# Optimization experiments

Hardware: AMD Instinct MI355X
Metric: run time of the kernel (lower is better)

## Reference

```python
import jax, jax.numpy as jnp
import numpy as np

B, T, D = 32, 1024, 1024  # batch, t_k (encoder steps), attn_sz == cell_state_sz


def setup_inputs() -> dict:
    key = jax.random.key(0)
    ks = jax.random.split(key, 7)
    scale = 1.0 / np.sqrt(D)
    return {
        "h_i": jax.random.normal(ks[0], (B, T, D), jnp.float32),
        "s_t": jax.random.normal(ks[1], (B, D), jnp.float32),
        "coverage": jax.random.uniform(ks[2], (B, T), jnp.float32),
        "W_h": jax.random.normal(ks[3], (D, D), jnp.float32) * scale,
        "W_s": jax.random.normal(ks[4], (D, D), jnp.float32) * scale,
        "b_s": jnp.zeros((D,), jnp.float32),
        "W_c": jax.random.normal(ks[5], (D,), jnp.float32) * scale,  # Dense(1 -> D) kernel
        "V_w": jax.random.normal(ks[6], (D,), jnp.float32) * scale,  # Dense(D -> 1) kernel
    }


def reference(h_i, s_t, coverage, W_h, W_s, b_s, W_c, V_w):
    # enc_features = W_h(h_i): (B, T, D)
    enc_features = jnp.einsum("btd,de->bte", h_i, W_h)
    # dec_features = W_s(s_t) broadcast over time: (B, 1, D)
    dec_features = (s_t @ W_s + b_s)[:, None, :]
    # coverage features: scalar coverage per step times (1->D) kernel
    cov_features = coverage[:, :, None] * W_c[None, None, :]
    features = enc_features + dec_features + cov_features
    # e_t = V(tanh(features)) squeezed to (B, T)
    e_t = jnp.einsum("btd,d->bt", jnp.tanh(features), V_w)
    a_t = jax.nn.softmax(e_t, axis=1)
    coverage_new = coverage + a_t
    # context = a_t @ h_i : (B, D)
    context_vector = jnp.einsum("bt,btd->bd", a_t, h_i)
    return context_vector, a_t, coverage_new
```

## Files before the change

### kernel.cpp

```cpp
#include <hip/hip_runtime.h>

#define B_ 32
#define T_ 1024
#define D_ 1024
#define M_ (B_ * T_)
#define NT_ 8
#define NT2 4
#define BM_ 128
#define BN_ 128
#define BK_ 64
#define NKT (D_ / BK_)
#define LSTR 72

#define FENCE_ALL() asm volatile("s_waitcnt vmcnt(0) lgkmcnt(0)" ::: "memory")

typedef __attribute__((ext_vector_type(8))) short short8;
typedef __attribute__((ext_vector_type(4))) float f32x4;

__device__ __forceinline__ unsigned f2bf(float f) {
    union { float f; unsigned u; } v; v.f = f;
    return (v.u + 0x7FFFu + ((v.u >> 16) & 1u)) >> 16;
}
__device__ __forceinline__ unsigned pack2(float a, float b) {
    return f2bf(a) | (f2bf(b) << 16);
}
__device__ __forceinline__ float bf2f(unsigned hi16) {
    union { unsigned u; float f; } v; v.u = hi16 << 16;
    return v.f;
}
__device__ __forceinline__ float fast_tanh(float x) {
    x = fminf(15.0f, fmaxf(-15.0f, x));
    float e = __expf(2.0f * x);
    return (e - 1.0f) * __fdividef(1.0f, e + 1.0f);
}

#define PREP_CONVH_BLKS 2048
#define PREP_CONVWT_BLKS 256
#define PREP_DEC_BLKS (B_ * 16)
__global__ __launch_bounds__(256) void prep_kernel(
    const float* __restrict__ h_i, uint4* __restrict__ h_bf4,
    const float* __restrict__ W_h, unsigned short* __restrict__ Wt,
    const float* __restrict__ s_t, const float* __restrict__ W_s,
    const float* __restrict__ b_s, float* __restrict__ dec_part)
{
    __shared__ float smem[64 * 65];
    const int bid = blockIdx.x;
    const int tid = threadIdx.x;
    if (bid < PREP_CONVH_BLKS) {
        const int idx = bid * 256 + tid;
        const int stride = PREP_CONVH_BLKS * 256;
        const int ngroups = M_ * D_ / 8;
        const float4* in4 = (const float4*)h_i;
        for (int g = idx; g < ngroups; g += stride) {
            const float4 a = in4[2 * g];
            const float4 b = in4[2 * g + 1];
            h_bf4[g] = make_uint4(pack2(a.x, a.y), pack2(a.z, a.w),
                                  pack2(b.x, b.y), pack2(b.z, b.w));
        }
    } else if (bid < PREP_CONVH_BLKS + PREP_CONVWT_BLKS) {
        const int tb = bid - PREP_CONVH_BLKS;
        float (*tile)[65] = (float (*)[65])smem;
        const int k0 = (tb & 15) * 64;
        const int n0 = (tb >> 4) * 64;
        const int tx = tid & 63, ty = tid >> 6;
#pragma unroll
        for (int r = 0; r < 16; ++r) {
            const int row = ty * 16 + r;
            tile[row][tx] = W_h[(size_t)(k0 + row) * D_ + n0 + tx];
        }
        __syncthreads();
#pragma unroll
        for (int r = 0; r < 16; ++r) {
            const int row = ty * 16 + r;
            Wt[(size_t)(n0 + row) * D_ + k0 + tx] = (unsigned short)f2bf(tile[tx][row]);
        }
    } else {
        const int db = bid - (PREP_CONVH_BLKS + PREP_CONVWT_BLKS);
        const int kc = db & 3;
        const int nc = (db >> 2) & 3;
        const int b  = db >> 4;
        const int d = nc * 256 + tid;
        const int k0 = kc * 256;
        float* s_lds = smem;
        s_lds[tid] = s_t[b * D_ + k0 + tid];
        __syncthreads();
        float acc = (kc == 0) ? b_s[d] : 0.f;
#pragma unroll 8
        for (int k = 0; k < 256; ++k) acc += s_lds[k] * W_s[(size_t)(k0 + k) * D_ + d];
        dec_part[kc * (B_ * D_) + b * D_ + d] = acc;
    }
}

__global__ __launch_bounds__(512, 2) void attn_gemm2(
    const unsigned short* __restrict__ h_bf, const unsigned short* __restrict__ wt_bf,
    const float* __restrict__ dec_part, const float* __restrict__ coverage,
    const float* __restrict__ W_c, const float* __restrict__ V_w,
    float* __restrict__ e_part)
{
    __shared__ __align__(16) unsigned short lds2[2][2][256 * 64];
    __shared__ float e_red[4][256];

    const int tid = threadIdx.x;
    const int nt2 = blockIdx.x >> 7;
    const int mt  = blockIdx.x & 127;
    const int m0 = mt * 256;
    const int n0 = nt2 * 256;
    const int bb = m0 >> 10;

    const int wave = tid >> 6;
    const int lane = tid & 63;
    const int wr = wave >> 2;
    const int wc = wave & 3;
    const int lr = lane & 15;
    const int lk = lane >> 4;

    f32x4 acc[8][4];
    const f32x4 fzero = {0.f, 0.f, 0.f, 0.f};
#pragma unroll
    for (int i = 0; i < 8; ++i)
#pragma unroll
        for (int j = 0; j < 4; ++j) acc[i][j] = fzero;

    const char* gA = (const char*)h_bf + (size_t)m0 * (D_ * 2);
    const char* gB = (const char*)wt_bf + (size_t)n0 * (D_ * 2);
    const int lrow8 = lane >> 3;
    const int scol = (((lane & 7) ^ lrow8) << 4);
    const int sw = (lr & 7) << 4;

#define GLOAD(mat, chunk, kt, buf)                                                 \
    {                                                                              \
        const int row_ = (chunk) * 8 + lrow8;                                      \
        const size_t goff_ = (size_t)row_ * (D_ * 2) + (size_t)(kt) * 128 + scol;  \
        __builtin_amdgcn_global_load_lds(                                          \
            (const __attribute__((address_space(1))) void*)(((mat) ? gB : gA) + goff_), \
            (__attribute__((address_space(3))) void*)((char*)lds2 +                \
                ((buf) * 2 + (mat)) * 32768 + (chunk) * 1024), 16, 0, 0);          \
    }
#define ST_BLO(buf, kt) { GLOAD(1, 2 * wave, kt, buf); GLOAD(1, 2 * wave + 1, kt, buf); }
#define ST_BHI(buf, kt) { GLOAD(1, 16 + 2 * wave, kt, buf); GLOAD(1, 16 + 2 * wave + 1, kt, buf); }
#define ST_AU(buf, kt, g)                                                          \
    { const int c_ = (wave < 4) ? ((g) * 4 + wave) : (16 + (g) * 4 + (wave - 4));  \
      GLOAD(0, c_, kt, buf); }

#define PH_BAR(N)                                                                  \
    asm volatile("s_waitcnt vmcnt(" #N ")" ::: "memory");                          \
    __builtin_amdgcn_s_barrier();                                                  \
    asm volatile("" ::: "memory")

#define LOADA(g)                                                                   \
    _Pragma("unroll")                                                              \
    for (int m = 0; m < 2; ++m)                                                    \
        _Pragma("unroll")                                                          \
        for (int kk = 0; kk < 2; ++kk)                                             \
            aA[m][kk] = *(const short8*)(ldsA +                                    \
                (wr * 128 + ((g) * 2 + m) * 16 + lr) * 128 +                       \
                ((kk * 64 + lk * 16) ^ sw));

#define MFMAQ(g)                                                                   \
    __builtin_amdgcn_s_setprio(1);                                                 \
    _Pragma("unroll")                                                              \
    for (int m = 0; m < 2; ++m)                                                    \
        _Pragma("unroll")                                                          \
        for (int ni = 0; ni < 4; ++ni)                                             \
            _Pragma("unroll")                                                      \
            for (int kk = 0; kk < 2; ++kk)                                         \
                acc[(g) * 2 + m][ni] = __builtin_amdgcn_mfma_f32_16x16x32_bf16(    \
                    aA[m][kk], bB[ni][kk], acc[(g) * 2 + m][ni], 0, 0, 0);         \
    __builtin_amdgcn_s_setprio(0);

    ST_BLO(0, 0); ST_BHI(0, 0);
    ST_AU(0, 0, 0); ST_AU(0, 0, 1); ST_AU(0, 0, 2); ST_AU(0, 0, 3);
    FENCE_ALL();
    __syncthreads();

    for (int kt = 0; kt < NKT; ++kt) {
        const int cur = kt & 1;
        const int nxt = cur ^ 1;
        const int ktn = (kt + 1) & (NKT - 1);
        const char* ldsA = (const char*)lds2 + (cur * 2 + 0) * 32768;
        const char* ldsB = (const char*)lds2 + (cur * 2 + 1) * 32768;

        short8 aA[2][2];
        short8 bB[4][2];

        PH_BAR(3);
#pragma unroll
        for (int ni = 0; ni < 4; ++ni)
#pragma unroll
            for (int kk = 0; kk < 2; ++kk)
                bB[ni][kk] = *(const short8*)(ldsB +
                    (wc * 64 + ni * 16 + lr) * 128 + ((kk * 64 + lk * 16) ^ sw));
        LOADA(0);
        ST_BLO(nxt, ktn);
        MFMAQ(0);

        PH_BAR(4);
        LOADA(1);
        ST_BHI(nxt, ktn);
        ST_AU(nxt, ktn, 0);
        MFMAQ(1);

        PH_BAR(5);
        LOADA(2);
        ST_AU(nxt, ktn, 1);
        ST_AU(nxt, ktn, 2);
        MFMAQ(2);

        PH_BAR(7);
        LOADA(3);
        ST_AU(nxt, ktn, 3);
        MFMAQ(3);
    }
#undef GLOAD
#undef ST_BLO
#undef ST_BHI
#undef ST_AU
#undef PH_BAR
#undef LOADA
#undef MFMAQ

    FENCE_ALL();
    __syncthreads();

    float esum[8][4];
    float covv[8][4];
#pragma unroll
    for (int mi = 0; mi < 8; ++mi)
#pragma unroll
        for (int r = 0; r < 4; ++r) {
            esum[mi][r] = 0.f;
            covv[mi][r] = coverage[m0 + wr * 128 + mi * 16 + lk * 4 + r];
        }
    const float* dp = dec_part + bb * D_;
#pragma unroll
    for (int ni = 0; ni < 4; ++ni) {
        const int n = n0 + wc * 64 + ni * 16 + lr;
        const float vw = V_w[n];
        const float dc = dp[n] + dp[B_ * D_ + n] + dp[2 * B_ * D_ + n] + dp[3 * B_ * D_ + n];
        const float wcv = W_c[n];
#pragma unroll
        for (int mi = 0; mi < 8; ++mi)
#pragma unroll
            for (int r = 0; r < 4; ++r) {
                const float f = acc[mi][ni][r] + dc + covv[mi][r] * wcv;
                esum[mi][r] += fast_tanh(f) * vw;
            }
    }
#pragma unroll
    for (int off = 1; off <= 8; off <<= 1)
#pragma unroll
        for (int mi = 0; mi < 8; ++mi)
#pragma unroll
            for (int r = 0; r < 4; ++r)
                esum[mi][r] += __shfl_xor(esum[mi][r], off, 64);

    if (lr == 0) {
#pragma unroll
        for (int mi = 0; mi < 8; ++mi)
#pragma unroll
            for (int r = 0; r < 4; ++r)
                e_red[wc][wr * 128 + mi * 16 + lk * 4 + r] = esum[mi][r];
    }
    FENCE_ALL();
    __syncthreads();
    if (tid < 256)
        e_part[(size_t)nt2 * M_ + m0 + tid] =
            e_red[0][tid] + e_red[1][tid] + e_red[2][tid] + e_red[3][tid];
}

__global__ __launch_bounds__(256) void post_kernel(
    const float* __restrict__ e_part, const float* __restrict__ coverage,
    const unsigned short* __restrict__ h_bf,
    float* __restrict__ a_out, float* __restrict__ cov_out,
    float* __restrict__ ctx_out)
{
    const int bid = blockIdx.x;
    const int b = bid >> 3;
    const int s = bid & 7;
    const int tid = threadIdx.x;
    __shared__ float a_lds[T_];
    __shared__ float redmx[4], redsum[4];
    __shared__ float cred[4][128];

    float e[4];
#pragma unroll
    for (int j = 0; j < 4; ++j) {
        const int t = tid + j * 256;
        float ssum = 0.f;
#pragma unroll
        for (int p = 0; p < NT2; ++p) ssum += e_part[(size_t)p * M_ + b * T_ + t];
        e[j] = ssum;
    }
    float mx = fmaxf(fmaxf(e[0], e[1]), fmaxf(e[2], e[3]));
#pragma unroll
    for (int off = 32; off > 0; off >>= 1) mx = fmaxf(mx, __shfl_xor(mx, off, 64));
    if ((tid & 63) == 0) redmx[tid >> 6] = mx;
    __syncthreads();
    mx = fmaxf(fmaxf(redmx[0], redmx[1]), fmaxf(redmx[2], redmx[3]));
    float p4[4];
    float ps = 0.f;
#pragma unroll
    for (int j = 0; j < 4; ++j) { p4[j] = __expf(e[j] - mx); ps += p4[j]; }
#pragma unroll
    for (int off = 32; off > 0; off >>= 1) ps += __shfl_xor(ps, off, 64);
    if ((tid & 63) == 0) redsum[tid >> 6] = ps;
    __syncthreads();
    ps = redsum[0] + redsum[1] + redsum[2] + redsum[3];
    const float inv = __fdividef(1.f, ps);
#pragma unroll
    for (int j = 0; j < 4; ++j) {
        const int t = tid + j * 256;
        const float a = p4[j] * inv;
        a_lds[t] = a;
        if (s == 0) {
            const int idx = b * T_ + t;
            a_out[idx] = a;
            cov_out[idx] = coverage[idx] + a;
        }
    }
    __syncthreads();

    const int dp = (tid & 63) * 2;
    const int q  = tid >> 6;
    const int d0 = s * 128 + dp;
    const unsigned short* hp = h_bf + ((size_t)(b * T_ + q * 256)) * D_ + d0;
    const float* al = a_lds + q * 256;
    float acc0 = 0.f, acc1 = 0.f;
#pragma unroll 8
    for (int t = 0; t < 256; ++t) {
        const unsigned v = *(const unsigned*)(hp + (size_t)t * D_);
        const float a = al[t];
        acc0 += a * bf2f(v & 0xFFFFu);
        acc1 += a * bf2f(v >> 16);
    }
    cred[q][dp] = acc0;
    cred[q][dp + 1] = acc1;
    __syncthreads();
    if (tid < 128)
        ctx_out[b * D_ + s * 128 + tid] =
            cred[0][tid] + cred[1][tid] + cred[2][tid] + cred[3][tid];
}

__global__ __launch_bounds__(256, 2) void attn_gemm_kernel(
    const float* __restrict__ h_i, const float* __restrict__ W_h,
    const float* __restrict__ dec_part, const float* __restrict__ coverage,
    const float* __restrict__ W_c, const float* __restrict__ V_w,
    float* __restrict__ e_part)
{
    __shared__ __align__(16) unsigned short lA[BM_][LSTR];
    __shared__ __align__(16) unsigned short lB[BN_][LSTR];
    __shared__ float e_red[256];

    const int tid = threadIdx.x;
    const int nt = blockIdx.x >> 8;
    const int mt = blockIdx.x & 255;
    const int m0 = mt * BM_;
    const int n0 = nt * BN_;
    const int bb = m0 >> 10;

    const int wave = tid >> 6;
    const int lane = tid & 63;
    const int wr = wave >> 1, wc = wave & 1;
    const int lr = lane & 15;
    const int lk = lane >> 4;

    f32x4 acc[4][4];
    const f32x4 fzero = {0.f, 0.f, 0.f, 0.f};
#pragma unroll
    for (int i = 0; i < 4; ++i)
#pragma unroll
        for (int j = 0; j < 4; ++j) acc[i][j] = fzero;

    const int a_row = tid >> 4;
    const int a_k = (tid & 15) << 2;
    const float* hA = h_i + (size_t)m0 * D_;

    for (int k0 = 0; k0 < D_; k0 += BK_) {
#pragma unroll
        for (int p = 0; p < 8; ++p) {
            const int row = a_row + p * 16;
            const float4 v = *(const float4*)(hA + (size_t)row * D_ + (k0 + a_k));
            *(uint2*)&lA[row][a_k] = make_uint2(pack2(v.x, v.y), pack2(v.z, v.w));
        }
#pragma unroll
        for (int p = 0; p < 8; ++p) {
            const int task = tid + p * 256;
            const int n = task & 127;
            const int kg = task >> 7;
            const float* wp = W_h + (size_t)(k0 + kg * 4) * D_ + n0 + n;
            const float x0 = wp[0 * D_], x1 = wp[1 * D_], x2 = wp[2 * D_], x3 = wp[3 * D_];
            *(uint2*)&lB[n][kg * 4] = make_uint2(pack2(x0, x1), pack2(x2, x3));
        }
        __syncthreads();

        short8 af[2][4], bfr[2][4];
#pragma unroll
        for (int kk = 0; kk < 2; ++kk)
#pragma unroll
            for (int i = 0; i < 4; ++i) {
                af[kk][i]  = *(const short8*)&lA[wr * 64 + i * 16 + lr][kk * 32 + lk * 8];
                bfr[kk][i] = *(const short8*)&lB[wc * 64 + i * 16 + lr][kk * 32 + lk * 8];
            }
#pragma unroll
        for (int kk = 0; kk < 2; ++kk)
#pragma unroll
            for (int mi = 0; mi < 4; ++mi)
#pragma unroll
                for (int ni = 0; ni < 4; ++ni)
                    acc[mi][ni] = __builtin_amdgcn_mfma_f32_16x16x32_bf16(
                        af[kk][mi], bfr[kk][ni], acc[mi][ni], 0, 0, 0);
        __syncthreads();
    }

    float esum[4][4];
    float covv[4][4];
#pragma unroll
    for (int mi = 0; mi < 4; ++mi)
#pragma unroll
        for (int r = 0; r < 4; ++r) {
            esum[mi][r] = 0.f;
            covv[mi][r] = coverage[m0 + wr * 64 + mi * 16 + lk * 4 + r];
        }
    const float* dp = dec_part + bb * D_;
#pragma unroll
    for (int ni = 0; ni < 4; ++ni) {
        const int n = n0 + wc * 64 + ni * 16 + lr;
        const float vw = V_w[n];
        const float dc = dp[n] + dp[B_ * D_ + n] + dp[2 * B_ * D_ + n] + dp[3 * B_ * D_ + n];
        const float wcv = W_c[n];
#pragma unroll
        for (int mi = 0; mi < 4; ++mi)
#pragma unroll
            for (int r = 0; r < 4; ++r) {
                const float f = acc[mi][ni][r] + dc + covv[mi][r] * wcv;
                esum[mi][r] += fast_tanh(f) * vw;
            }
    }
#pragma unroll
    for (int off = 1; off <= 8; off <<= 1)
#pragma unroll
        for (int mi = 0; mi < 4; ++mi)
#pragma unroll
            for (int r = 0; r < 4; ++r)
                esum[mi][r] += __shfl_xor(esum[mi][r], off, 64);

    if (lr == 0) {
#pragma unroll
        for (int mi = 0; mi < 4; ++mi)
#pragma unroll
            for (int r = 0; r < 4; ++r)
                e_red[wc * 128 + wr * 64 + mi * 16 + lk * 4 + r] = esum[mi][r];
    }
    __syncthreads();
    if (tid < 128)
        e_part[(size_t)nt * M_ + m0 + tid] = e_red[tid] + e_red[128 + tid];
}

__global__ __launch_bounds__(256) void softmax_kernel(
    const float* __restrict__ e_part, const float* __restrict__ coverage,
    float* __restrict__ a_out, float* __restrict__ cov_out,
    float* __restrict__ a_ws, int nparts)
{
    const int b = blockIdx.x;
    const int tid = threadIdx.x;
    __shared__ float redmx[4], redsum[4];
    float e[4];
#pragma unroll
    for (int j = 0; j < 4; ++j) {
        const int t = tid + j * 256;
        float ssum = 0.f;
        for (int p = 0; p < nparts; ++p) ssum += e_part[(size_t)p * M_ + b * T_ + t];
        e[j] = ssum;
    }
    float mx = fmaxf(fmaxf(e[0], e[1]), fmaxf(e[2], e[3]));
#pragma unroll
    for (int off = 32; off > 0; off >>= 1) mx = fmaxf(mx, __shfl_xor(mx, off, 64));
    if ((tid & 63) == 0) redmx[tid >> 6] = mx;
    __syncthreads();
    mx = fmaxf(fmaxf(redmx[0], redmx[1]), fmaxf(redmx[2], redmx[3]));
    float p4[4];
    float ps = 0.f;
#pragma unroll
    for (int j = 0; j < 4; ++j) { p4[j] = __expf(e[j] - mx); ps += p4[j]; }
#pragma unroll
    for (int off = 32; off > 0; off >>= 1) ps += __shfl_xor(ps, off, 64);
    if ((tid & 63) == 0) redsum[tid >> 6] = ps;
    __syncthreads();
    ps = redsum[0] + redsum[1] + redsum[2] + redsum[3];
    const float inv = __fdividef(1.f, ps);
#pragma unroll
    for (int j = 0; j < 4; ++j) {
        const int idx = b * T_ + tid + j * 256;
        const float a = p4[j] * inv;
        a_out[idx] = a;
        a_ws[idx] = a;
        cov_out[idx] = coverage[idx] + a;
    }
}

__global__ __launch_bounds__(256) void ctx_part_f32(
    const float* __restrict__ h_i, const float* __restrict__ a_t,
    float* __restrict__ ctx_part)
{
    const int bid = blockIdx.x;
    const int b = bid >> 4;
    const int dc = (bid >> 2) & 3;
    const int tc = bid & 3;
    const int tid = threadIdx.x;
    const int d = dc * 256 + tid;
    __shared__ float a_lds[256];
    a_lds[tid] = a_t[b * T_ + tc * 256 + tid];
    __syncthreads();
    const float* hp = h_i + ((size_t)(b * T_ + tc * 256)) * D_ + d;
    float acc = 0.f;
#pragma unroll 8
    for (int t = 0; t < 256; ++t) acc += a_lds[t] * hp[(size_t)t * D_];
    ctx_part[tc * (B_ * D_) + b * D_ + d] = acc;
}

__global__ __launch_bounds__(256) void dec_kernel(
    const float* __restrict__ s_t, const float* __restrict__ W_s,
    const float* __restrict__ b_s, float* __restrict__ dec_part)
{
    const int bid = blockIdx.x;
    const int kc = bid & 3;
    const int nc = (bid >> 2) & 3;
    const int b  = bid >> 4;
    const int d = nc * 256 + threadIdx.x;
    const int k0 = kc * 256;
    __shared__ float s_lds[256];
    s_lds[threadIdx.x] = s_t[b * D_ + k0 + threadIdx.x];
    __syncthreads();
    float acc = (kc == 0) ? b_s[d] : 0.f;
#pragma unroll 8
    for (int k = 0; k < 256; ++k) acc += s_lds[k] * W_s[(size_t)(k0 + k) * D_ + d];
    dec_part[kc * (B_ * D_) + b * D_ + d] = acc;
}

__global__ __launch_bounds__(256) void ctx_reduce_kernel(
    const float* __restrict__ ctx_part, float* __restrict__ out)
{
    const int i = blockIdx.x * 256 + threadIdx.x;
    out[i] = ctx_part[i] + ctx_part[B_ * D_ + i] + ctx_part[2 * B_ * D_ + i] +
             ctx_part[3 * B_ * D_ + i];
}

extern "C" void kernel_launch(void* const* d_in, const int* in_sizes, int n_in,
                              void* d_out, int out_size, void* d_ws, size_t ws_size,
                              hipStream_t stream)
{
    (void)in_sizes; (void)n_in; (void)out_size;
    const float* h_i      = (const float*)d_in[0];
    const float* s_t      = (const float*)d_in[1];
    const float* coverage = (const float*)d_in[2];
    const float* W_h      = (const float*)d_in[3];
    const float* W_s      = (const float*)d_in[4];
    const float* b_s      = (const float*)d_in[5];
    const float* W_c      = (const float*)d_in[6];
    const float* V_w      = (const float*)d_in[7];

    float* out     = (float*)d_out;
    float* ctx_out = out;
    float* a_out   = out + B_ * T_;
    float* cov_out = out + 2 * B_ * T_;

    float* ws       = (float*)d_ws;
    float* dec_part = ws;
    float* e_part   = dec_part + 4 * B_ * D_;
    float* ctx_part = e_part + NT_ * M_;
    float* a_ws     = ctx_part + 4 * B_ * D_;
    const size_t f32_count = 8 * (size_t)B_ * D_ + (size_t)NT_ * M_ + (size_t)B_ * T_;
    unsigned short* h_bf  = (unsigned short*)(ws + f32_count);
    unsigned short* wt_bf = h_bf + (size_t)M_ * D_;
    const size_t need = f32_count * 4 + ((size_t)M_ * D_ + (size_t)D_ * D_) * 2;

    if (ws_size >= need) {
        prep_kernel<<<PREP_CONVH_BLKS + PREP_CONVWT_BLKS + PREP_DEC_BLKS, 256, 0, stream>>>(
            h_i, (uint4*)h_bf, W_h, wt_bf, s_t, W_s, b_s, dec_part);
        attn_gemm2<<<NT2 * (M_ / 256), 512, 0, stream>>>(h_bf, wt_bf, dec_part,
                                                         coverage, W_c, V_w, e_part);
        post_kernel<<<B_ * 8, 256, 0, stream>>>(e_part, coverage, h_bf,
                                                a_out, cov_out, ctx_out);
    } else {
        dec_kernel<<<B_ * 16, 256, 0, stream>>>(s_t, W_s, b_s, dec_part);
        attn_gemm_kernel<<<NT_ * (M_ / BM_), 256, 0, stream>>>(h_i, W_h, dec_part,
                                                               coverage, W_c, V_w, e_part);
        softmax_kernel<<<B_, 256, 0, stream>>>(e_part, coverage, a_out, cov_out, a_ws, NT_);
        ctx_part_f32<<<B_ * 16, 256, 0, stream>>>(h_i, a_ws, ctx_part);
        ctx_reduce_kernel<<<(B_ * D_) / 256, 256, 0, stream>>>(ctx_part, ctx_out);
    }
}
```

Before: 135.5 us.

## Fuse fp32-to-bf16 conversion of h_i into GEMM A-tile loading

Removes the separate pass that converted all of h_i to a bf16 workspace copy. The GEMM now loads fp32 A tiles into registers, packs them to bf16 and writes them to LDS, with B prefetched two stages ahead via direct-to-LDS loads. The post kernel reads fp32 h_i directly with 512 threads. This saves a full read/write sweep of h_i but doubles per-tile A read bytes across the four N-tiles and adds register pressure and VALU conversion work inside the GEMM loop.

```diff
diff --git a/kernel.cpp b/kernel.cpp
--- a/kernel.cpp
+++ b/kernel.cpp
@@ -24,21 +24,15 @@
 __device__ __forceinline__ unsigned pack2(float a, float b) {
     return f2bf(a) | (f2bf(b) << 16);
 }
-__device__ __forceinline__ float bf2f(unsigned hi16) {
-    union { unsigned u; float f; } v; v.u = hi16 << 16;
-    return v.f;
-}
 __device__ __forceinline__ float fast_tanh(float x) {
     x = fminf(15.0f, fmaxf(-15.0f, x));
     float e = __expf(2.0f * x);
     return (e - 1.0f) * __fdividef(1.0f, e + 1.0f);
 }
 
-#define PREP_CONVH_BLKS 2048
 #define PREP_CONVWT_BLKS 256
 #define PREP_DEC_BLKS (B_ * 16)
 __global__ __launch_bounds__(256) void prep_kernel(
-    const float* __restrict__ h_i, uint4* __restrict__ h_bf4,
     const float* __restrict__ W_h, unsigned short* __restrict__ Wt,
     const float* __restrict__ s_t, const float* __restrict__ W_s,
     const float* __restrict__ b_s, float* __restrict__ dec_part)
@@ -46,22 +40,10 @@
     __shared__ float smem[64 * 65];
     const int bid = blockIdx.x;
     const int tid = threadIdx.x;
-    if (bid < PREP_CONVH_BLKS) {
-        const int idx = bid * 256 + tid;
-        const int stride = PREP_CONVH_BLKS * 256;
-        const int ngroups = M_ * D_ / 8;
-        const float4* in4 = (const float4*)h_i;
-        for (int g = idx; g < ngroups; g += stride) {
-            const float4 a = in4[2 * g];
-            const float4 b = in4[2 * g + 1];
-            h_bf4[g] = make_uint4(pack2(a.x, a.y), pack2(a.z, a.w),
-                                  pack2(b.x, b.y), pack2(b.z, b.w));
-        }
-    } else if (bid < PREP_CONVH_BLKS + PREP_CONVWT_BLKS) {
-        const int tb = bid - PREP_CONVH_BLKS;
+    if (bid < PREP_CONVWT_BLKS) {
         float (*tile)[65] = (float (*)[65])smem;
-        const int k0 = (tb & 15) * 64;
-        const int n0 = (tb >> 4) * 64;
+        const int k0 = (bid & 15) * 64;
+        const int n0 = (bid >> 4) * 64;
         const int tx = tid & 63, ty = tid >> 6;
 #pragma unroll
         for (int r = 0; r < 16; ++r) {
@@ -75,7 +57,7 @@
             Wt[(size_t)(n0 + row) * D_ + k0 + tx] = (unsigned short)f2bf(tile[tx][row]);
         }
     } else {
-        const int db = bid - (PREP_CONVH_BLKS + PREP_CONVWT_BLKS);
+        const int db = bid - PREP_CONVWT_BLKS;
         const int kc = db & 3;
         const int nc = (db >> 2) & 3;
         const int b  = db >> 4;
@@ -91,8 +73,8 @@
     }
 }
 
-__global__ __launch_bounds__(512, 2) void attn_gemm2(
-    const unsigned short* __restrict__ h_bf, const unsigned short* __restrict__ wt_bf,
+__global__ __launch_bounds__(512, 2) void attn_gemm3(
+    const float* __restrict__ h_i, const unsigned short* __restrict__ wt_bf,
     const float* __restrict__ dec_part, const float* __restrict__ coverage,
     const float* __restrict__ W_c, const float* __restrict__ V_w,
     float* __restrict__ e_part)
@@ -121,29 +103,56 @@
 #pragma unroll
         for (int j = 0; j < 4; ++j) acc[i][j] = fzero;
 
-    const char* gA = (const char*)h_bf + (size_t)m0 * (D_ * 2);
+    const float* gAf = h_i + (size_t)m0 * D_;
     const char* gB = (const char*)wt_bf + (size_t)n0 * (D_ * 2);
     const int lrow8 = lane >> 3;
     const int scol = (((lane & 7) ^ lrow8) << 4);
     const int sw = (lr & 7) << 4;
 
-#define GLOAD(mat, chunk, kt, buf)                                                 \
+    float4 aP[4][2];
+
+#define CHUNKOF(g) ((wave < 4) ? ((g) * 4 + wave) : (16 + (g) * 4 + (wave - 4)))
+
+#define GLOADB(chunk, kt, buf)                                                     \
+    __builtin_amdgcn_global_load_lds(                                              \
+        (const __attribute__((address_space(1))) void*)(gB +                       \
+            (size_t)((chunk) * 8 + lrow8) * (D_ * 2) + (size_t)(kt) * 128 + scol), \
+        (__attribute__((address_space(3))) void*)((char*)lds2 +                    \
+            ((buf) * 2 + 1) * 32768 + (chunk) * 1024), 16, 0, 0);
+
+#define BSTAGE(buf, kt)                                                            \
+    { GLOADB(2 * wave, kt, buf); GLOADB(2 * wave + 1, kt, buf);                    \
+      GLOADB(16 + 2 * wave, kt, buf); GLOADB(16 + 2 * wave + 1, kt, buf); }
+
+#define ALOADS(kt)                                                                 \
     {                                                                              \
-        const int row_ = (chunk) * 8 + lrow8;                                      \
-        const size_t goff_ = (size_t)row_ * (D_ * 2) + (size_t)(kt) * 128 + scol;  \
-        __builtin_amdgcn_global_load_lds(                                          \
-            (const __attribute__((address_space(1))) void*)(((mat) ? gB : gA) + goff_), \
-            (__attribute__((address_space(3))) void*)((char*)lds2 +                \
-                ((buf) * 2 + (mat)) * 32768 + (chunk) * 1024), 16, 0, 0);          \
-    }
-#define ST_BLO(buf, kt) { GLOAD(1, 2 * wave, kt, buf); GLOAD(1, 2 * wave + 1, kt, buf); }
-#define ST_BHI(buf, kt) { GLOAD(1, 16 + 2 * wave, kt, buf); GLOAD(1, 16 + 2 * wave + 1, kt, buf); }
-#define ST_AU(buf, kt, g)                                                          \
-    { const int c_ = (wave < 4) ? ((g) * 4 + wave) : (16 + (g) * 4 + (wave - 4));  \
-      GLOAD(0, c_, kt, buf); }
+        _Pragma("unroll")                                                          \
+        for (int g = 0; g < 4; ++g) {                                              \
+            const float* p_ = gAf + (size_t)(CHUNKOF(g) * 8 + lrow8) * D_ +        \
+                              (kt) * 64 + (scol >> 1);                             \
+            aP[g][0] = *(const float4*)p_;                                         \
+            aP[g][1] = *(const float4*)(p_ + 4);                                   \
+        }                                                                          \
+    }
+
+#define AWRITE(g, bufn)                                                            \
+    {                                                                              \
+        uint4 w_;                                                                  \
+        w_.x = pack2(aP[g][0].x, aP[g][0].y);                                      \
+        w_.y = pack2(aP[g][0].z, aP[g][0].w);                                      \
+        w_.z = pack2(aP[g][1].x, aP[g][1].y);                                      \
+        w_.w = pack2(aP[g][1].z, aP[g][1].w);                                      \
+        *(uint4*)((char*)lds2 + ((bufn) * 2 + 0) * 32768 +                         \
+                  CHUNKOF(g) * 1024 + lane * 16) = w_;                             \
+    }
 
 #define PH_BAR(N)                                                                  \
-    asm volatile("s_waitcnt vmcnt(" #N ")" ::: "memory");                          \
+    asm volatile("s_waitcnt vmcnt(" #N ") lgkmcnt(0)" ::: "memory");               \
+    __builtin_amdgcn_s_barrier();                                                  \
+    asm volatile("" ::: "memory")
+
+#define LG_BAR()                                                                   \
+    asm volatile("s_waitcnt lgkmcnt(0)" ::: "memory");                             \
     __builtin_amdgcn_s_barrier();                                                  \
     asm volatile("" ::: "memory")
 
@@ -168,22 +177,26 @@
                     aA[m][kk], bB[ni][kk], acc[(g) * 2 + m][ni], 0, 0, 0);         \
     __builtin_amdgcn_s_setprio(0);
 
-    ST_BLO(0, 0); ST_BHI(0, 0);
-    ST_AU(0, 0, 0); ST_AU(0, 0, 1); ST_AU(0, 0, 2); ST_AU(0, 0, 3);
-    FENCE_ALL();
-    __syncthreads();
+    BSTAGE(0, 0);
+    BSTAGE(1, 1);
+    ALOADS(0);
+    asm volatile("s_waitcnt vmcnt(0)" ::: "memory");
+    AWRITE(0, 0); AWRITE(1, 0); AWRITE(2, 0); AWRITE(3, 0);
+    ALOADS(1);
+    asm volatile("s_waitcnt lgkmcnt(0)" ::: "memory");
+    __builtin_amdgcn_s_barrier();
 
     for (int kt = 0; kt < NKT; ++kt) {
         const int cur = kt & 1;
         const int nxt = cur ^ 1;
-        const int ktn = (kt + 1) & (NKT - 1);
+        const int kp2 = (kt + 2) & (NKT - 1);
         const char* ldsA = (const char*)lds2 + (cur * 2 + 0) * 32768;
         const char* ldsB = (const char*)lds2 + (cur * 2 + 1) * 32768;
 
         short8 aA[2][2];
         short8 bB[4][2];
 
-        PH_BAR(3);
+        PH_BAR(20);
 #pragma unroll
         for (int ni = 0; ni < 4; ++ni)
 #pragma unroll
@@ -191,31 +204,31 @@
                 bB[ni][kk] = *(const short8*)(ldsB +
                     (wc * 64 + ni * 16 + lr) * 128 + ((kk * 64 + lk * 16) ^ sw));
         LOADA(0);
-        ST_BLO(nxt, ktn);
         MFMAQ(0);
 
+        LG_BAR();
+        LOADA(1);
+        BSTAGE(cur, kp2);
+        MFMAQ(1);
+
+        PH_BAR(8);
+        LOADA(2);
+        AWRITE(0, nxt); AWRITE(1, nxt);
+        MFMAQ(2);
+
         PH_BAR(4);
-        LOADA(1);
-        ST_BHI(nxt, ktn);
-        ST_AU(nxt, ktn, 0);
-        MFMAQ(1);
-
-        PH_BAR(5);
-        LOADA(2);
-        ST_AU(nxt, ktn, 1);
-        ST_AU(nxt, ktn, 2);
-        MFMAQ(2);
-
-        PH_BAR(7);
         LOADA(3);
-        ST_AU(nxt, ktn, 3);
+        AWRITE(2, nxt); AWRITE(3, nxt);
+        ALOADS(kp2);
         MFMAQ(3);
     }
-#undef GLOAD
-#undef ST_BLO
-#undef ST_BHI
-#undef ST_AU
+#undef CHUNKOF
+#undef GLOADB
+#undef BSTAGE
+#undef ALOADS
+#undef AWRITE
 #undef PH_BAR
+#undef LG_BAR
 #undef LOADA
 #undef MFMAQ
 
@@ -268,9 +281,9 @@
             e_red[0][tid] + e_red[1][tid] + e_red[2][tid] + e_red[3][tid];
 }
 
-__global__ __launch_bounds__(256) void post_kernel(
+__global__ __launch_bounds__(512) void post_kernel(
     const float* __restrict__ e_part, const float* __restrict__ coverage,
-    const unsigned short* __restrict__ h_bf,
+    const float* __restrict__ h_i,
     float* __restrict__ a_out, float* __restrict__ cov_out,
     float* __restrict__ ctx_out)
 {
@@ -279,66 +292,65 @@
     const int s = bid & 7;
     const int tid = threadIdx.x;
     __shared__ float a_lds[T_];
-    __shared__ float redmx[4], redsum[4];
-    __shared__ float cred[4][128];
-
-    float e[4];
-#pragma unroll
-    for (int j = 0; j < 4; ++j) {
-        const int t = tid + j * 256;
-        float ssum = 0.f;
-#pragma unroll
-        for (int p = 0; p < NT2; ++p) ssum += e_part[(size_t)p * M_ + b * T_ + t];
-        e[j] = ssum;
-    }
-    float mx = fmaxf(fmaxf(e[0], e[1]), fmaxf(e[2], e[3]));
+    __shared__ float redmx[8], redsum[8];
+    __shared__ float cred[8][128];
+
+    float e0 = 0.f, e1 = 0.f;
+#pragma unroll
+    for (int p = 0; p < NT2; ++p) {
+        e0 += e_part[(size_t)p * M_ + b * T_ + tid];
+        e1 += e_part[(size_t)p * M_ + b * T_ + tid + 512];
+    }
+    float mx = fmaxf(e0, e1);
 #pragma unroll
     for (int off = 32; off > 0; off >>= 1) mx = fmaxf(mx, __shfl_xor(mx, off, 64));
     if ((tid & 63) == 0) redmx[tid >> 6] = mx;
     __syncthreads();
-    mx = fmaxf(fmaxf(redmx[0], redmx[1]), fmaxf(redmx[2], redmx[3]));
-    float p4[4];
-    float ps = 0.f;
-#pragma unroll
-    for (int j = 0; j < 4; ++j) { p4[j] = __expf(e[j] - mx); ps += p4[j]; }
+    mx = redmx[0];
+#pragma unroll
+    for (int w = 1; w < 8; ++w) mx = fmaxf(mx, redmx[w]);
+    const float p0 = __expf(e0 - mx);
+    const float p1 = __expf(e1 - mx);
+    float ps = p0 + p1;
 #pragma unroll
     for (int off = 32; off > 0; off >>= 1) ps += __shfl_xor(ps, off, 64);
     if ((tid & 63) == 0) redsum[tid >> 6] = ps;
     __syncthreads();
-    ps = redsum[0] + redsum[1] + redsum[2] + redsum[3];
+    ps = redsum[0] + redsum[1] + redsum[2] + redsum[3] +
+         redsum[4] + redsum[5] + redsum[6] + redsum[7];
     const float inv = __fdividef(1.f, ps);
-#pragma unroll
-    for (int j = 0; j < 4; ++j) {
-        const int t = tid + j * 256;
-        const float a = p4[j] * inv;
-        a_lds[t] = a;
-        if (s == 0) {
-            const int idx = b * T_ + t;
-            a_out[idx] = a;
-            cov_out[idx] = coverage[idx] + a;
-        }
+    const float a0 = p0 * inv, a1 = p1 * inv;
+    a_lds[tid] = a0;
+    a_lds[tid + 512] = a1;
+    if (s == 0) {
+        const int i0 = b * T_ + tid;
+        a_out[i0] = a0;
+        cov_out[i0] = coverage[i0] + a0;
+        a_out[i0 + 512] = a1;
+        cov_out[i0 + 512] = coverage[i0 + 512] + a1;
     }
     __syncthreads();
 
     const int dp = (tid & 63) * 2;
     const int q  = tid >> 6;
     const int d0 = s * 128 + dp;
-    const unsigned short* hp = h_bf + ((size_t)(b * T_ + q * 256)) * D_ + d0;
-    const float* al = a_lds + q * 256;
+    const float* hp = h_i + ((size_t)(b * T_ + q * 128)) * D_ + d0;
+    const float* al = a_lds + q * 128;
     float acc0 = 0.f, acc1 = 0.f;
-#pragma unroll 8
-    for (int t = 0; t < 256; ++t) {
-        const unsigned v = *(const unsigned*)(hp + (size_t)t * D_);
+#pragma unroll 4
+    for (int t = 0; t < 128; ++t) {
+        const float2 v = *(const float2*)(hp + (size_t)t * D_);
         const float a = al[t];
-        acc0 += a * bf2f(v & 0xFFFFu);
-        acc1 += a * bf2f(v >> 16);
+        acc0 += a * v.x;
+        acc1 += a * v.y;
     }
     cred[q][dp] = acc0;
     cred[q][dp + 1] = acc1;
     __syncthreads();
     if (tid < 128)
         ctx_out[b * D_ + s * 128 + tid] =
-            cred[0][tid] + cred[1][tid] + cred[2][tid] + cred[3][tid];
+            cred[0][tid] + cred[1][tid] + cred[2][tid] + cred[3][tid] +
+            cred[4][tid] + cred[5][tid] + cred[6][tid] + cred[7][tid];
 }
 
 __global__ __launch_bounds__(256, 2) void attn_gemm_kernel(
@@ -570,16 +582,15 @@
     float* ctx_part = e_part + NT_ * M_;
     float* a_ws     = ctx_part + 4 * B_ * D_;
     const size_t f32_count = 8 * (size_t)B_ * D_ + (size_t)NT_ * M_ + (size_t)B_ * T_;
-    unsigned short* h_bf  = (unsigned short*)(ws + f32_count);
-    unsigned short* wt_bf = h_bf + (size_t)M_ * D_;
-    const size_t need = f32_count * 4 + ((size_t)M_ * D_ + (size_t)D_ * D_) * 2;
+    unsigned short* wt_bf = (unsigned short*)(ws + f32_count);
+    const size_t need = f32_count * 4 + (size_t)D_ * D_ * 2;
 
     if (ws_size >= need) {
-        prep_kernel<<<PREP_CONVH_BLKS + PREP_CONVWT_BLKS + PREP_DEC_BLKS, 256, 0, stream>>>(
-            h_i, (uint4*)h_bf, W_h, wt_bf, s_t, W_s, b_s, dec_part);
-        attn_gemm2<<<NT2 * (M_ / 256), 512, 0, stream>>>(h_bf, wt_bf, dec_part,
+        prep_kernel<<<PREP_CONVWT_BLKS + PREP_DEC_BLKS, 256, 0, stream>>>(
+            W_h, wt_bf, s_t, W_s, b_s, dec_part);
+        attn_gemm3<<<NT2 * (M_ / 256), 512, 0, stream>>>(h_i, wt_bf, dec_part,
                                                          coverage, W_c, V_w, e_part);
-        post_kernel<<<B_ * 8, 256, 0, stream>>>(e_part, coverage, h_bf,
+        post_kernel<<<B_ * 8, 512, 0, stream>>>(e_part, coverage, h_i,
                                                 a_out, cov_out, ctx_out);
     } else {
         dec_kernel<<<B_ * 16, 256, 0, stream>>>(s_t, W_s, b_s, dec_part);
```

Result: slower. 189.9 us (+40.2%).
